# Performance work log

Measured on AMD Instinct MI355X. Metric: run time of the kernel, lower is better.

## Reference

```python
import jax, jax.numpy as jnp
import numpy as np

N = 100000
E = 1600000
D = 128


def setup_inputs() -> dict:
    key = jax.random.key(0)
    ks = jax.random.split(key, 6)
    x = jax.random.normal(ks[0], (N, D), dtype=jnp.float32)
    edge_row = jax.random.randint(ks[1], (E,), 0, N)
    edge_col = jax.random.randint(ks[2], (E,), 0, N)
    edge_val = jax.random.uniform(ks[3], (E,), dtype=jnp.float32)
    # Kaiming-ish init for the MLP weights
    W1 = jax.random.normal(ks[4], (D, D), dtype=jnp.float32) * (1.0 / np.sqrt(D))
    W2 = jax.random.normal(ks[5], (D, D), dtype=jnp.float32) * (1.0 / np.sqrt(D))
    b1 = jnp.zeros((D,), dtype=jnp.float32)
    b2 = jnp.zeros((D,), dtype=jnp.float32)
    eps = jnp.zeros((1,), dtype=jnp.float32)  # GIN eps, init 0
    bias = jnp.zeros((D,), dtype=jnp.float32)
    return {"x": x, "edge_row": edge_row, "edge_col": edge_col, "edge_val": edge_val,
            "W1": W1, "b1": b1, "W2": W2, "b2": b2, "eps": eps, "bias": bias}


def reference(x, edge_row, edge_col, edge_val, W1, b1, W2, b2, eps, bias):
    # sparse adj @ x : out[i] = sum_{edges (i,j)} val * x[j]
    agg = jax.ops.segment_sum(edge_val[:, None] * x[edge_col], edge_row, num_segments=N)
    h = (1.0 + eps) * x + agg                     # eps-scaled residual, [N, D]
    h = jax.nn.relu(h @ W1 + b1)                  # MLP layer 1
    h = jax.nn.relu(h @ W2 + b2)                  # MLP layer 2
    out = jax.nn.relu(h + bias)                   # bias + final relu
    return out
```

## Files before the change

kernel.cpp:

```cpp
#include <hip/hip_runtime.h>
#include <stdint.h>


static constexpr int NN = 100000;
static constexpr int NE = 1600000;
static constexpr int NB = 392;
static constexpr int EPB = 4096;
static constexpr int PB = (NE + EPB - 1) / EPB;
static constexpr int BCAP = 8192;

typedef float f32x4 __attribute__((ext_vector_type(4)));
typedef short s16x8 __attribute__((ext_vector_type(8)));

__device__ __forceinline__ uint16_t f2bf(float f) {
  uint32_t u = __float_as_uint(f);
  u += 0x7fffu + ((u >> 16) & 1u);
  return (uint16_t)(u >> 16);
}
__device__ __forceinline__ float2 bf2f(uint32_t w) {
  float2 r;
  r.x = __uint_as_float(w << 16);
  r.y = __uint_as_float(w & 0xffff0000u);
  return r;
}

template <int WIDTH>
__device__ __forceinline__ int* scan_inc(int* s0, int* s1, int tid) {
  int* pin = s0;
  int* pout = s1;
  for (int off = 1; off < WIDTH; off <<= 1) {
    if (tid < WIDTH) pout[tid] = pin[tid] + ((tid >= off) ? pin[tid - off] : 0);
    __syncthreads();
    int* tmp = pin; pin = pout; pout = tmp;
  }
  return pin;
}

__global__ __launch_bounds__(256) void k_cvt(const float* __restrict__ x,
                                             uint32_t* __restrict__ xb, int nq,
                                             int* __restrict__ btot,
                                             int2* __restrict__ es_pad) {
  int i = blockIdx.x * 256 + threadIdx.x;
  if (i < nq) {
    float4 v = ((const float4*)x)[i];
    uint2 o;
    o.x = (uint32_t)f2bf(v.x) | ((uint32_t)f2bf(v.y) << 16);
    o.y = (uint32_t)f2bf(v.z) | ((uint32_t)f2bf(v.w) << 16);
    ((uint2*)xb)[i] = o;
  }
  if (blockIdx.x == 0) {
    int t = threadIdx.x;
    for (int j = t; j < NB; j += 256) btot[j] = 0;
    if (t < 8) es_pad[t] = int2{0, 0};
  }
}

__global__ __launch_bounds__(1024) void k_part(const int* __restrict__ erow,
                                               const int* __restrict__ ecol,
                                               const float* __restrict__ eval,
                                               int2* __restrict__ part,
                                               int* __restrict__ runstart,
                                               int* __restrict__ bucket_tot) {
  __shared__ int hist[NB];
  __shared__ int cur[NB];
  __shared__ int s0[512], s1[512];
  __shared__ int2 stage[EPB];
  int t = threadIdx.x;
  int base = blockIdx.x * EPB;
  int cnt = min(EPB, NE - base);

  if (t < NB) hist[t] = 0;
  __syncthreads();

  int pb[4], pk[4], pv[4];
  #pragma unroll
  for (int j = 0; j < 4; ++j) {
    int i = t + j * 1024;
    pb[j] = -1;
    if (i < cnt) {
      int e = base + i;
      int r = erow[e];
      int b = r >> 8;
      pb[j] = b;
      pk[j] = ecol[e] | ((r & 255) << 17);
      pv[j] = __float_as_int(eval[e]);
      atomicAdd(&hist[b], 1);
    }
  }
  __syncthreads();

  if (t < 512) s0[t] = (t < NB) ? hist[t] : 0;
  __syncthreads();
  int* inc = scan_inc<512>(s0, s1, t);

  if (t < NB) {
    int h = hist[t];
    int st = inc[t] - h;
    cur[t] = st;
    runstart[blockIdx.x * (NB + 1) + t] = st;
    atomicAdd(&bucket_tot[t], h);
  }
  if (t == 0) runstart[blockIdx.x * (NB + 1) + NB] = cnt;
  __syncthreads();

  #pragma unroll
  for (int j = 0; j < 4; ++j) {
    if (pb[j] >= 0) {
      int off = atomicAdd(&cur[pb[j]], 1);
      stage[off] = int2{pk[j], pv[j]};
    }
  }
  __syncthreads();

  for (int i = t; i < cnt; i += 1024) part[base + i] = stage[i];
}

__global__ __launch_bounds__(1024) void k_bucket(const int2* __restrict__ part,
                                                 const int* __restrict__ runstart,
                                                 const int* __restrict__ btot,
                                                 int2* __restrict__ es,
                                                 int* __restrict__ rowptr) {
  __shared__ int cum[PB + 1];
  __shared__ int rbas[PB];
  __shared__ int hist[256];
  __shared__ int rps[256];
  __shared__ int cur[256];
  __shared__ int s0[512], s1[512];
  __shared__ int sbase;
  __shared__ int2 stage[BCAP];
  int b = blockIdx.x, t = threadIdx.x;

  int bt = (t < NB) ? btot[t] : 0;
  if (t < 512) s0[t] = bt;
  __syncthreads();
  {
    int* incb = scan_inc<512>(s0, s1, t);
    if (t == b) sbase = incb[b] - bt;
  }
  __syncthreads();
  int base_out = sbase;

  int len = 0;
  if (t < PB) {
    int rs = runstart[t * (NB + 1) + b];
    int re = runstart[t * (NB + 1) + b + 1];
    len = re - rs;
    rbas[t] = t * EPB + rs;
  }
  __syncthreads();
  if (t < 512) s0[t] = (t < PB) ? len : 0;
  __syncthreads();
  int* inc1 = scan_inc<512>(s0, s1, t);
  if (t < PB) cum[t] = inc1[t] - len;
  if (t == 0) cum[PB] = inc1[PB - 1];
  if (t < 256) hist[t] = 0;
  __syncthreads();

  int total = cum[PB];

  int pk[8], pv[8];
  #pragma unroll
  for (int j = 0; j < 8; ++j) {
    int s = t + j * 1024;
    pk[j] = -1;
    if (s < total) {
      int lo = 0, hi = PB;
      while (hi - lo > 1) {
        int mid = (lo + hi) >> 1;
        if (cum[mid] <= s) lo = mid; else hi = mid;
      }
      int2 ev = part[rbas[lo] + (s - cum[lo])];
      pk[j] = ev.x; pv[j] = ev.y;
      atomicAdd(&hist[ev.x >> 17], 1);
    }
  }
  __syncthreads();

  if (t < 256) s0[t] = hist[t];
  __syncthreads();
  int* inc2 = scan_inc<256>(s0, s1, t);
  if (t < 256) {
    int ex = inc2[t] - hist[t];
    rps[t] = ex;
    cur[t] = ex;
  }
  __syncthreads();

  if (t < 256) {
    int row = b * 256 + t;
    if (row <= NN) rowptr[row] = base_out + rps[t];
  }

  #pragma unroll
  for (int j = 0; j < 8; ++j) {
    if (pk[j] >= 0) {
      int rib = pk[j] >> 17;
      int off = atomicAdd(&cur[rib], 1);
      int2 rec = int2{pk[j] & 0x1FFFF, pv[j]};
      if (off < BCAP) stage[off] = rec;
      else es[base_out + off] = rec;
    }
  }
  __syncthreads();

  for (int i = t; i < total; i += 1024) es[base_out + i] = stage[i];
}

__global__ __launch_bounds__(256) void k_agg(const uint32_t* __restrict__ xb,
                                             const int2* __restrict__ es,
                                             const int* __restrict__ rowptr,
                                             const float* __restrict__ eps,
                                             uint32_t* __restrict__ hb) {
  int wid = (blockIdx.x * 256 + threadIdx.x) >> 6;
  int wave = __builtin_amdgcn_readfirstlane(wid);
  int lane = threadIdx.x & 63;
  float e = 1.0f + eps[0];
  float2 h = bf2f(xb[(size_t)wave * 64 + lane]);
  h.x *= e; h.y *= e;
  int beg = __builtin_amdgcn_readfirstlane(rowptr[wave]);
  int end = __builtin_amdgcn_readfirstlane(rowptr[wave + 1]);
  for (int k = beg; k < end; k += 8) {
    int scol[8]; float sval[8];
    #pragma unroll
    for (int j = 0; j < 8; ++j) {
      int2 ev = es[k + j];
      scol[j] = __builtin_amdgcn_readfirstlane(ev.x);
      int vb = __builtin_amdgcn_readfirstlane(ev.y);
      sval[j] = (k + j < end) ? __int_as_float(vb) : 0.0f;
    }
    uint32_t xw[8];
    #pragma unroll
    for (int j = 0; j < 8; ++j)
      xw[j] = xb[((size_t)scol[j] << 6) + lane];
    #pragma unroll
    for (int j = 0; j < 8; ++j) {
      float2 xv = bf2f(xw[j]);
      h.x = fmaf(sval[j], xv.x, h.x);
      h.y = fmaf(sval[j], xv.y, h.y);
    }
  }
  hb[(size_t)wave * 64 + lane] = (uint32_t)f2bf(h.x) | ((uint32_t)f2bf(h.y) << 16);
}

__global__ __launch_bounds__(256, 3) void k_mlp(const uint16_t* __restrict__ A,
                                                const float* __restrict__ W1,
                                                const float* __restrict__ b1,
                                                const float* __restrict__ W2,
                                                const float* __restrict__ b2,
                                                const float* __restrict__ bias,
                                                float* __restrict__ out, int nrows) {
  __shared__ uint16_t wt[128 * 136];
  __shared__ uint16_t h1[64 * 136];
  int tid = threadIdx.x;

  #pragma unroll 4
  for (int it = 0; it < 64; ++it) {
    int idx = tid + it * 256;
    wt[(idx & 127) * 136 + (idx >> 7)] = f2bf(W1[idx]);
  }
  __syncthreads();

  int wv = tid >> 6, l = tid & 63;
  int m16 = l & 15, qg = l >> 4;
  int r0 = blockIdx.x * 64 + wv * 16;
  int arow = r0 + m16;
  if (arow >= nrows) arow = nrows - 1;

  f32x4 acc[8];
  #pragma unroll
  for (int n0 = 0; n0 < 8; ++n0) acc[n0] = f32x4{0.f, 0.f, 0.f, 0.f};

  #pragma unroll
  for (int k0 = 0; k0 < 128; k0 += 32) {
    s16x8 a = *(const s16x8*)(A + (size_t)arow * 128 + k0 + qg * 8);
    #pragma unroll
    for (int n0 = 0; n0 < 8; ++n0) {
      s16x8 bfr = *(const s16x8*)(&wt[(n0 * 16 + m16) * 136 + k0 + qg * 8]);
      acc[n0] = __builtin_amdgcn_mfma_f32_16x16x32_bf16(a, bfr, acc[n0], 0, 0, 0);
    }
  }

  #pragma unroll
  for (int n0 = 0; n0 < 8; ++n0) {
    int col = n0 * 16 + m16;
    float bb = b1[col];
    #pragma unroll
    for (int j = 0; j < 4; ++j) {
      int lr = wv * 16 + qg * 4 + j;
      h1[lr * 136 + col] = f2bf(fmaxf(acc[n0][j] + bb, 0.0f));
    }
  }
  __syncthreads();

  #pragma unroll 4
  for (int it = 0; it < 64; ++it) {
    int idx = tid + it * 256;
    wt[(idx & 127) * 136 + (idx >> 7)] = f2bf(W2[idx]);
  }
  #pragma unroll
  for (int n0 = 0; n0 < 8; ++n0) acc[n0] = f32x4{0.f, 0.f, 0.f, 0.f};
  __syncthreads();

  #pragma unroll
  for (int k0 = 0; k0 < 128; k0 += 32) {
    s16x8 a = *(const s16x8*)(&h1[(wv * 16 + m16) * 136 + k0 + qg * 8]);
    #pragma unroll
    for (int n0 = 0; n0 < 8; ++n0) {
      s16x8 bfr = *(const s16x8*)(&wt[(n0 * 16 + m16) * 136 + k0 + qg * 8]);
      acc[n0] = __builtin_amdgcn_mfma_f32_16x16x32_bf16(a, bfr, acc[n0], 0, 0, 0);
    }
  }

  #pragma unroll
  for (int n0 = 0; n0 < 8; ++n0) {
    int col = n0 * 16 + m16;
    float bb = b2[col];
    float b3 = bias[col];
    #pragma unroll
    for (int j = 0; j < 4; ++j) {
      int row = r0 + qg * 4 + j;
      if (row < nrows) {
        float v = fmaxf(fmaxf(acc[n0][j] + bb, 0.0f) + b3, 0.0f);
        out[(size_t)row * 128 + col] = v;
      }
    }
  }
}

extern "C" void kernel_launch(void* const* d_in, const int* in_sizes, int n_in,
                              void* d_out, int out_size, void* d_ws, size_t ws_size,
                              hipStream_t stream) {
  const float* x    = (const float*)d_in[0];
  const int*   erow = (const int*)d_in[1];
  const int*   ecol = (const int*)d_in[2];
  const float* eval = (const float*)d_in[3];
  const float* W1   = (const float*)d_in[4];
  const float* b1   = (const float*)d_in[5];
  const float* W2   = (const float*)d_in[6];
  const float* b2   = (const float*)d_in[7];
  const float* eps  = (const float*)d_in[8];
  const float* bias = (const float*)d_in[9];

  char* w = (char*)d_ws;
  size_t off = 0;
  auto take = [&](size_t bytes) -> void* {
    void* p = w + off;
    off = (off + bytes + 255) & ~(size_t)255;
    return p;
  };
  uint32_t* xb     = (uint32_t*)take((size_t)NN * 64 * 4);
  uint32_t* hb     = (uint32_t*)take((size_t)NN * 64 * 4);
  int2*     part   = (int2*)take((size_t)NE * 8);
  int2*     es     = (int2*)take((size_t)(NE + 8) * 8);
  int*      rowptr = (int*)take((size_t)(NN + 1) * 4);
  int*      runst  = (int*)take((size_t)PB * (NB + 1) * 4);
  int*      btot   = (int*)take((size_t)(NB + 1) * 4);
  (void)ws_size;

  k_cvt<<<(NN * 32 + 255) / 256, 256, 0, stream>>>(x, xb, NN * 32, btot, es + NE);
  k_part<<<PB, 1024, 0, stream>>>(erow, ecol, eval, part, runst, btot);
  k_bucket<<<NB, 1024, 0, stream>>>(part, runst, btot, es, rowptr);
  k_agg<<<(NN + 3) / 4, 256, 0, stream>>>(xb, es, rowptr, eps, hb);
  k_mlp<<<(NN + 63) / 64, 256, 0, stream>>>((const uint16_t*)hb, W1, b1, W2, b2,
                                            bias, (float*)d_out, NN);
}
```

Before: 256.1 us.

## Merge x conversion into partition kernel and pre-convert MLP weights to bf16

The separate bf16 conversion kernel is folded into the edge-partition kernel as extra blocks, so the conversion and the partitioning run concurrently in one launch. Those extra blocks also convert W1 and W2 once into a transposed, packed bf16 buffer. Each MLP block then loads its weights with vectorized 16-byte copies instead of doing 64 strided fp32 loads and conversions per block. Buffer zeroing moves to memset calls, which adds two small stream operations. The merged kernel's 1024-thread blocks with large shared memory may schedule the conversion work less efficiently.

```diff
diff --git a/kernel.cpp b/kernel.cpp
--- a/kernel.cpp
+++ b/kernel.cpp
@@ -8,6 +8,8 @@
 static constexpr int EPB = 4096;
 static constexpr int PB = (NE + EPB - 1) / EPB;
 static constexpr int BCAP = 8192;
+static constexpr int NCVT = (NN * 32) / 1024;
+static constexpr int NWB = 16;
 
 typedef float f32x4 __attribute__((ext_vector_type(4)));
 typedef short s16x8 __attribute__((ext_vector_type(8)));
@@ -36,37 +38,50 @@
   return pin;
 }
 
-__global__ __launch_bounds__(256) void k_cvt(const float* __restrict__ x,
-                                             uint32_t* __restrict__ xb, int nq,
-                                             int* __restrict__ btot,
-                                             int2* __restrict__ es_pad) {
-  int i = blockIdx.x * 256 + threadIdx.x;
-  if (i < nq) {
-    float4 v = ((const float4*)x)[i];
-    uint2 o;
-    o.x = (uint32_t)f2bf(v.x) | ((uint32_t)f2bf(v.y) << 16);
-    o.y = (uint32_t)f2bf(v.z) | ((uint32_t)f2bf(v.w) << 16);
-    ((uint2*)xb)[i] = o;
-  }
-  if (blockIdx.x == 0) {
-    int t = threadIdx.x;
-    for (int j = t; j < NB; j += 256) btot[j] = 0;
-    if (t < 8) es_pad[t] = int2{0, 0};
-  }
-}
-
-__global__ __launch_bounds__(1024) void k_part(const int* __restrict__ erow,
+__global__ __launch_bounds__(1024) void k_prep(const float* __restrict__ x,
+                                               uint32_t* __restrict__ xb,
+                                               const int* __restrict__ erow,
                                                const int* __restrict__ ecol,
                                                const float* __restrict__ eval,
                                                int2* __restrict__ part,
                                                int* __restrict__ runstart,
-                                               int* __restrict__ bucket_tot) {
+                                               int* __restrict__ bucket_tot,
+                                               const float* __restrict__ W1,
+                                               const float* __restrict__ W2,
+                                               uint32_t* __restrict__ wbp) {
   __shared__ int hist[NB];
   __shared__ int cur[NB];
   __shared__ int s0[512], s1[512];
   __shared__ int2 stage[EPB];
   int t = threadIdx.x;
-  int base = blockIdx.x * EPB;
+  int bid = blockIdx.x;
+
+  if (bid >= PB) {
+    int cid = bid - PB;
+    if (cid < NCVT) {
+      int i = cid * 1024 + t;
+      if (i < NN * 32) {
+        float4 v = ((const float4*)x)[i];
+        uint2 o;
+        o.x = (uint32_t)f2bf(v.x) | ((uint32_t)f2bf(v.y) << 16);
+        o.y = (uint32_t)f2bf(v.z) | ((uint32_t)f2bf(v.w) << 16);
+        ((uint2*)xb)[i] = o;
+      }
+    } else {
+      int flat = (cid - NCVT) * 1024 + t;
+      int m = flat >> 13;
+      int p = flat & 8191;
+      int n = p >> 6;
+      int k = (p & 63) * 2;
+      const float* Wm = m ? W2 : W1;
+      uint32_t lo = f2bf(Wm[k * 128 + n]);
+      uint32_t hi = f2bf(Wm[(k + 1) * 128 + n]);
+      wbp[(size_t)m * 8192 + n * 64 + (p & 63)] = lo | (hi << 16);
+    }
+    return;
+  }
+
+  int base = bid * EPB;
   int cnt = min(EPB, NE - base);
 
   if (t < NB) hist[t] = 0;
@@ -97,10 +112,10 @@
     int h = hist[t];
     int st = inc[t] - h;
     cur[t] = st;
-    runstart[blockIdx.x * (NB + 1) + t] = st;
+    runstart[bid * (NB + 1) + t] = st;
     atomicAdd(&bucket_tot[t], h);
   }
-  if (t == 0) runstart[blockIdx.x * (NB + 1) + NB] = cnt;
+  if (t == 0) runstart[bid * (NB + 1) + NB] = cnt;
   __syncthreads();
 
   #pragma unroll
@@ -243,9 +258,8 @@
 }
 
 __global__ __launch_bounds__(256, 3) void k_mlp(const uint16_t* __restrict__ A,
-                                                const float* __restrict__ W1,
+                                                const uint16_t* __restrict__ wb,
                                                 const float* __restrict__ b1,
-                                                const float* __restrict__ W2,
                                                 const float* __restrict__ b2,
                                                 const float* __restrict__ bias,
                                                 float* __restrict__ out, int nrows) {
@@ -253,10 +267,11 @@
   __shared__ uint16_t h1[64 * 136];
   int tid = threadIdx.x;
 
-  #pragma unroll 4
-  for (int it = 0; it < 64; ++it) {
-    int idx = tid + it * 256;
-    wt[(idx & 127) * 136 + (idx >> 7)] = f2bf(W1[idx]);
+  #pragma unroll
+  for (int it = 0; it < 8; ++it) {
+    int c = tid + it * 256;
+    int r = c >> 4, cc = c & 15;
+    *(uint4*)&wt[r * 136 + cc * 8] = *(const uint4*)&wb[r * 128 + cc * 8];
   }
   __syncthreads();
 
@@ -292,10 +307,11 @@
   }
   __syncthreads();
 
-  #pragma unroll 4
-  for (int it = 0; it < 64; ++it) {
-    int idx = tid + it * 256;
-    wt[(idx & 127) * 136 + (idx >> 7)] = f2bf(W2[idx]);
+  #pragma unroll
+  for (int it = 0; it < 8; ++it) {
+    int c = tid + it * 256;
+    int r = c >> 4, cc = c & 15;
+    *(uint4*)&wt[r * 136 + cc * 8] = *(const uint4*)&wb[16384 + r * 128 + cc * 8];
   }
   #pragma unroll
   for (int n0 = 0; n0 < 8; ++n0) acc[n0] = f32x4{0.f, 0.f, 0.f, 0.f};
@@ -355,12 +371,17 @@
   int*      rowptr = (int*)take((size_t)(NN + 1) * 4);
   int*      runst  = (int*)take((size_t)PB * (NB + 1) * 4);
   int*      btot   = (int*)take((size_t)(NB + 1) * 4);
+  uint32_t* wb     = (uint32_t*)take((size_t)2 * 8192 * 4);
   (void)ws_size;
 
-  k_cvt<<<(NN * 32 + 255) / 256, 256, 0, stream>>>(x, xb, NN * 32, btot, es + NE);
-  k_part<<<PB, 1024, 0, stream>>>(erow, ecol, eval, part, runst, btot);
+  hipMemsetAsync(btot, 0, (size_t)(NB + 1) * 4, stream);
+  hipMemsetAsync(es + NE, 0, (size_t)8 * 8, stream);
+
+  k_prep<<<PB + NCVT + NWB, 1024, 0, stream>>>(x, xb, erow, ecol, eval, part,
+                                               runst, btot, W1, W2, wb);
   k_bucket<<<NB, 1024, 0, stream>>>(part, runst, btot, es, rowptr);
   k_agg<<<(NN + 3) / 4, 256, 0, stream>>>(xb, es, rowptr, eps, hb);
-  k_mlp<<<(NN + 63) / 64, 256, 0, stream>>>((const uint16_t*)hb, W1, b1, W2, b2,
+  k_mlp<<<(NN + 63) / 64, 256, 0, stream>>>((const uint16_t*)hb,
+                                            (const uint16_t*)wb, b1, b2,
                                             bias, (float*)d_out, NN);
 }
```

Measured after the change: 242.0 us. 1.06x faster.
